# Kernel tuning notes

Measured on AMD Instinct MI355X. Metric: run time of the kernel, lower is better.

## Reference

```python
import jax, jax.numpy as jnp
import numpy as np

D_IN, D_OUT, D_K, D_V, H = 768, 768, 64, 64, 12


def setup_inputs() -> dict:
    key = jax.random.key(0)
    ks = jax.random.split(key, 16)
    b, nq, nk = 4, 1024, 1024
    inp = {
        'queries': jax.random.normal(ks[0], (b, nq, D_IN), jnp.float32),
        'keys': jax.random.normal(ks[1], (b, nk, D_IN), jnp.float32),
        'values': jax.random.normal(ks[2], (b, nk, D_IN), jnp.float32),
        'loss_map': jax.random.normal(ks[3], (b, nk, H), jnp.float32),
        'attention_mask': jax.random.randint(ks[4], (b, H, nq, nk), 0, 2).astype(bool),
        'attention_weights': jax.random.uniform(ks[5], (b, H, nq, nk), jnp.float32),
        # learned params (stored as (in, out); math-equivalent to torch Linear)
        'Wq': jax.random.normal(ks[6], (D_IN, H * D_K), jnp.float32) * 0.02,
        'bq': jnp.zeros((H * D_K,), jnp.float32),
        'Wk': jax.random.normal(ks[7], (D_IN, H * D_K), jnp.float32) * 0.02,
        'bk': jnp.zeros((H * D_K,), jnp.float32),
        'Wv': jax.random.normal(ks[8], (D_IN, H * D_V), jnp.float32) * 0.02,
        'bv': jnp.zeros((H * D_V,), jnp.float32),
        'Wo': jax.random.normal(ks[9], (H * D_V, D_OUT), jnp.float32) * 0.02,
        'bo': jnp.zeros((D_OUT,), jnp.float32),
    }
    return inp


def reference(queries, keys, values, loss_map, attention_mask, attention_weights,
              Wq, bq, Wk, bk, Wv, bv, Wo, bo):
    b, nq, _ = queries.shape
    nk = keys.shape[1]
    # projections -> (b, h, n, d)
    q = (queries @ Wq + bq).reshape(b, nq, H, D_K).transpose(0, 2, 1, 3)
    k = (keys @ Wk + bk).reshape(b, nk, H, D_K).transpose(0, 2, 1, 3)
    v = (values @ Wv + bv).reshape(b, nk, H, D_V).transpose(0, 2, 1, 3)
    # scaled scores (b, h, nq, nk)
    att = jnp.einsum('bhqd,bhkd->bhqk', q, k) / np.sqrt(D_K).astype(np.float32)
    att = att * attention_weights
    att = jnp.where(attention_mask, -jnp.inf, att)
    # additive per-key, per-head bias: loss_map (b, nk, h) -> (b, h, 1, nk)
    w_g = loss_map.transpose(0, 2, 1)[:, :, None, :]
    w_mn = jax.nn.softmax(att + w_g, axis=-1)
    # dropout is identity in eval / p=0
    out = jnp.einsum('bhqk,bhkd->bhqd', w_mn, v)
    out = out.transpose(0, 2, 1, 3).reshape(b, nq, H * D_V)
    return out @ Wo + bo
```

## Files before the change

### kernel.cpp

```cpp
#include <hip/hip_runtime.h>
#include <hip/hip_bf16.h>
#include <hip/hip_fp16.h>
#include <cmath>

static constexpr int HN = 12;
static constexpr int DHEAD = 64;
static constexpr int DMODEL = 768;
static constexpr int NQ = 1024;
static constexpr int NB = 4;
static constexpr int NCH = 4;
static constexpr int MROWS = NB * NQ;
static constexpr size_t PER = (size_t)NB * HN * NQ * DHEAD;
static constexpr size_t WN  = (size_t)DMODEL * DMODEL;
static constexpr size_t CHROWS = (size_t)NB * HN * NQ;

typedef __attribute__((ext_vector_type(8))) short bf16x8;
typedef __attribute__((ext_vector_type(4))) float f32x4;

static __device__ __forceinline__ unsigned short f2bf(float f) {
    unsigned int u = __builtin_bit_cast(unsigned int, f);
    unsigned int r = (u + 0x7FFFu + ((u >> 16) & 1u)) >> 16;
    return (unsigned short)r;
}
static __device__ __forceinline__ unsigned pack2(float lo, float hi) {
    return (unsigned)f2bf(lo) | ((unsigned)f2bf(hi) << 16);
}
static __device__ __forceinline__ unsigned short f2h(float f) {
    return __half_as_ushort(__float2half(f));
}

typedef const __attribute__((address_space(1))) unsigned int gu32;
typedef __attribute__((address_space(3))) unsigned int lu32;
static __device__ __forceinline__ void gload16(const void* g, void* l) {
    __builtin_amdgcn_global_load_lds((gu32*)g, (lu32*)l, 16, 0, 0);
}

__global__ __launch_bounds__(256)
void cvt3(const float* __restrict__ a, const float* __restrict__ b, const float* __restrict__ c,
          unsigned short* __restrict__ oa, unsigned short* __restrict__ ob, unsigned short* __restrict__ oc)
{
    const int z = blockIdx.z;
    const float* s = z == 0 ? a : z == 1 ? b : c;
    unsigned short* d = z == 0 ? oa : z == 1 ? ob : oc;
    size_t i = ((size_t)blockIdx.x * 256 + threadIdx.x) * 4;
    float4 v = *(const float4*)&s[i];
    ushort4 u;
    u.x = f2bf(v.x); u.y = f2bf(v.y); u.z = f2bf(v.z); u.w = f2bf(v.w);
    *(ushort4*)&d[i] = u;
}

__global__ __launch_bounds__(256)
void wtrans(const float* __restrict__ w0, const float* __restrict__ w1,
            const float* __restrict__ w2, const float* __restrict__ w3,
            unsigned short* __restrict__ o0, unsigned short* __restrict__ o1,
            unsigned short* __restrict__ o2, unsigned short* __restrict__ o3)
{
    const int z = blockIdx.z;
    const float* in = z == 0 ? w0 : z == 1 ? w1 : z == 2 ? w2 : w3;
    unsigned short* out = z == 0 ? o0 : z == 1 ? o1 : z == 2 ? o2 : o3;
    __shared__ float t[64][65];
    const int tid = threadIdx.x;
    const int k0 = blockIdx.x * 64, n0 = blockIdx.y * 64;
    #pragma unroll
    for (int l = 0; l < 16; ++l) {
        int idx = l * 256 + tid, r = idx >> 6, cc = idx & 63;
        t[r][cc] = in[(size_t)(k0 + r) * DMODEL + n0 + cc];
    }
    __syncthreads();
    #pragma unroll
    for (int l = 0; l < 16; ++l) {
        int idx = l * 256 + tid, r = idx >> 6, cc = idx & 63;
        out[(size_t)(n0 + r) * DMODEL + k0 + cc] = f2bf(t[cc][r]);
    }
}

static __device__ __forceinline__
void gemm_body(const unsigned short* __restrict__ A, const unsigned short* __restrict__ Wt,
               const float* __restrict__ bias, void* __restrict__ C, int layout)
{
    constexpr int K = DMODEL;
    __shared__ unsigned short As[128 * 64];
    __shared__ unsigned short Bs[128 * 64];
    const int tid = threadIdx.x, w = tid >> 6, lane = tid & 63;
    const int c = lane & 15, g = lane >> 4;
    const int wr = w >> 1, wc = w & 1;
    const int bn = blockIdx.x * 128, bm = blockIdx.y * 128;

    f32x4 acc[4][4] = {};
    for (int k0 = 0; k0 < K; k0 += 64) {
        #pragma unroll
        for (int it = 0; it < 4; ++it) {
            int idx = it * 256 + tid, r = idx >> 3, blk = idx & 7;
            int so = (blk ^ (r & 7)) << 3;
            gload16(A  + (size_t)(bm + r) * K + k0 + so, &As[(it * 256 + w * 64) * 8]);
            gload16(Wt + (size_t)(bn + r) * K + k0 + so, &Bs[(it * 256 + w * 64) * 8]);
        }
        __syncthreads();
        #pragma unroll
        for (int kk = 0; kk < 2; ++kk) {
            bf16x8 a[4], b[4];
            #pragma unroll
            for (int mi = 0; mi < 4; ++mi) {
                int row = wr * 64 + mi * 16 + c;
                a[mi] = *(const bf16x8*)&As[row * 64 + ((((kk << 2) | g) ^ (row & 7)) << 3)];
            }
            #pragma unroll
            for (int ni = 0; ni < 4; ++ni) {
                int row = wc * 64 + ni * 16 + c;
                b[ni] = *(const bf16x8*)&Bs[row * 64 + ((((kk << 2) | g) ^ (row & 7)) << 3)];
            }
            #pragma unroll
            for (int mi = 0; mi < 4; ++mi)
                #pragma unroll
                for (int ni = 0; ni < 4; ++ni)
                    acc[mi][ni] = __builtin_amdgcn_mfma_f32_16x16x32_bf16(a[mi], b[ni], acc[mi][ni], 0, 0, 0);
        }
        __syncthreads();
    }

    #pragma unroll
    for (int ni = 0; ni < 4; ++ni) {
        int col = bn + wc * 64 + ni * 16 + c;
        float bvx = bias[col];
        int hh = col >> 6, d = col & 63;
        #pragma unroll
        for (int mi = 0; mi < 4; ++mi) {
            int m0 = bm + wr * 64 + mi * 16 + 4 * g;
            int bb = m0 >> 10, nn0 = m0 & (NQ - 1);
            if (layout == 0) {
                float* o = (float*)C;
                #pragma unroll
                for (int j = 0; j < 4; ++j)
                    o[(size_t)(m0 + j) * DMODEL + col] = acc[mi][ni][j] + bvx;
            } else if (layout == 1) {
                unsigned short* o = (unsigned short*)C;
                #pragma unroll
                for (int j = 0; j < 4; ++j)
                    o[(((size_t)bb * HN + hh) * NQ + nn0 + j) * DHEAD + d] =
                        f2bf(acc[mi][ni][j] + bvx);
            } else {
                unsigned short* o = (unsigned short*)C;
                ushort4 u;
                u.x = f2bf(acc[mi][ni][0] + bvx);
                u.y = f2bf(acc[mi][ni][1] + bvx);
                u.z = f2bf(acc[mi][ni][2] + bvx);
                u.w = f2bf(acc[mi][ni][3] + bvx);
                *(ushort4*)&o[(((size_t)bb * HN + hh) * DHEAD + d) * NQ + nn0] = u;
            }
        }
    }
}

__global__ __launch_bounds__(256)
void qkv_gemm(const unsigned short* __restrict__ qa, const unsigned short* __restrict__ ka,
              const unsigned short* __restrict__ va,
              const unsigned short* __restrict__ wq, const unsigned short* __restrict__ wk,
              const unsigned short* __restrict__ wv,
              const float* __restrict__ bq, const float* __restrict__ bk, const float* __restrict__ bv,
              unsigned short* __restrict__ qo, unsigned short* __restrict__ ko,
              unsigned short* __restrict__ vo)
{
    const int z = blockIdx.z;
    const unsigned short* A  = z == 0 ? qa : z == 1 ? ka : va;
    const unsigned short* Wt = z == 0 ? wq : z == 1 ? wk : wv;
    const float* bias        = z == 0 ? bq : z == 1 ? bk : bv;
    unsigned short* C        = z == 0 ? qo : z == 1 ? ko : vo;
    gemm_body(A, Wt, bias, C, z == 2 ? 2 : 1);
}

__global__ __launch_bounds__(256)
void o_gemm(const unsigned short* __restrict__ A, const unsigned short* __restrict__ Wt,
            const float* __restrict__ bias, float* __restrict__ C)
{
    gemm_body(A, Wt, bias, C, 0);
}

__global__ __launch_bounds__(256, 5)
void attn_part(const unsigned short* __restrict__ qws,
               const unsigned short* __restrict__ kws,
               const unsigned short* __restrict__ vtws,
               const float* __restrict__ aw, const int* __restrict__ mask,
               const float* __restrict__ lm,
               unsigned short* __restrict__ opart, float* __restrict__ mpart,
               float* __restrict__ lpart)
{
    const int qt = blockIdx.x, h = blockIdx.y;
    const int b = blockIdx.z >> 2, ch = blockIdx.z & 3;
    const int tid = threadIdx.x;
    const int w = tid >> 6, lane = tid & 63;
    const int c = lane & 15, g = lane >> 4;

    __shared__ unsigned short Ks[2][32 * 64];
    __shared__ unsigned short Vs[2][64 * 32];
    __shared__ float lms[256];

    const size_t bh = (size_t)b * HN + h;
    const unsigned short* qbase  = qws  + (bh * NQ + (size_t)qt * 64) * DHEAD;
    const unsigned short* kbase  = kws  + (bh * NQ + (size_t)ch * 256) * DHEAD;
    const unsigned short* vtbase = vtws + bh * DHEAD * NQ + ch * 256;

    auto stageKV = [&](int kt, int bufi) {
        {
            int r = tid >> 3, blk = tid & 7;
            int so = (blk ^ (r & 7)) << 3;
            gload16(kbase + (size_t)(kt * 32 + r) * DHEAD + so, &Ks[bufi][(w * 64) * 8]);
        }
        {
            int r = tid >> 2, blk = tid & 3;
            int so = ((blk ^ ((tid >> 4) & 3)) << 3);
            gload16(vtbase + (size_t)r * NQ + kt * 32 + so, &Vs[bufi][(w * 64) * 8]);
        }
    };

    const int qrow = w * 16 + c;
    const bf16x8 qf0 = *(const bf16x8*)&qbase[qrow * DHEAD + g * 8];
    const bf16x8 qf1 = *(const bf16x8*)&qbase[qrow * DHEAD + 32 + g * 8];

    const size_t awbase = (bh * NQ + (size_t)(qt * 64 + qrow)) * NQ + ch * 256;

    f32x4 O[4] = {{0,0,0,0},{0,0,0,0},{0,0,0,0},{0,0,0,0}};
    float mrun = -1e30f, lrun = 0.f;
    const int srcl = c + ((g & 1) << 5);
    const bool hiT = (g >> 1) != 0;
    const int vsw = (c >> 2);

    lms[tid] = lm[((size_t)b * NQ + ch * 256 + tid) * HN + h];
    stageKV(0, 0);
    __syncthreads();

    #pragma unroll
    for (int kt = 0; kt < 8; ++kt) {
        const int cur = kt & 1;
        if (kt < 7) stageKV(kt + 1, cur ^ 1);

        float4 aw4[2]; int4 mk4[2]; float4 lm4[2];
        #pragma unroll
        for (int nt = 0; nt < 2; ++nt) {
            size_t o = awbase + kt * 32 + nt * 16 + 4 * g;
            aw4[nt] = *(const float4*)&aw[o];
            mk4[nt] = *(const int4*)&mask[o];
            lm4[nt] = *(const float4*)&lms[kt * 32 + nt * 16 + 4 * g];
        }

        f32x4 s[2] = {{0,0,0,0},{0,0,0,0}};
        #pragma unroll
        for (int kk = 0; kk < 2; ++kk) {
            bf16x8 qf = kk ? qf1 : qf0;
            #pragma unroll
            for (int nt = 0; nt < 2; ++nt) {
                int krow = nt * 16 + c;
                bf16x8 kf = *(const bf16x8*)&Ks[cur][krow * 64 + ((((kk << 2) | g) ^ (c & 7)) << 3)];
                s[nt] = __builtin_amdgcn_mfma_f32_16x16x32_bf16(kf, qf, s[nt], 0, 0, 0);
            }
        }

        float p[2][4];
        float tmax = -INFINITY;
        #pragma unroll
        for (int nt = 0; nt < 2; ++nt) {
            const float* av = (const float*)&aw4[nt];
            const int*   mv = (const int*)&mk4[nt];
            const float* lv = (const float*)&lm4[nt];
            #pragma unroll
            for (int j = 0; j < 4; ++j) {
                float v = mv[j] ? -1e30f : fmaf(s[nt][j], 0.125f * av[j], lv[j]);
                p[nt][j] = v;
                tmax = fmaxf(tmax, v);
            }
        }
        tmax = fmaxf(tmax, __shfl_xor(tmax, 16));
        tmax = fmaxf(tmax, __shfl_xor(tmax, 32));

        float mn = fmaxf(mrun, tmax);
        float scal = __expf(mrun - mn);
        mrun = mn;
        float rs = 0.f;
        #pragma unroll
        for (int nt = 0; nt < 2; ++nt)
            #pragma unroll
            for (int j = 0; j < 4; ++j) {
                float e = __expf(p[nt][j] - mn);
                p[nt][j] = e;
                rs += e;
            }
        rs += __shfl_xor(rs, 16);
        rs += __shfl_xor(rs, 32);
        lrun = lrun * scal + rs;
        #pragma unroll
        for (int nd = 0; nd < 4; ++nd) O[nd] *= scal;

        int pk[2][2];
        #pragma unroll
        for (int nt = 0; nt < 2; ++nt) {
            pk[nt][0] = (int)pack2(p[nt][0], p[nt][1]);
            pk[nt][1] = (int)pack2(p[nt][2], p[nt][3]);
        }

        {
            int xa0 = __shfl(pk[0][0], srcl),      xb0 = __shfl(pk[1][0], srcl);
            int xa1 = __shfl(pk[0][1], srcl),      xb1 = __shfl(pk[1][1], srcl);
            int xa2 = __shfl(pk[0][0], srcl + 16), xb2 = __shfl(pk[1][0], srcl + 16);
            int xa3 = __shfl(pk[0][1], srcl + 16), xb3 = __shfl(pk[1][1], srcl + 16);
            int4 bi;
            bi.x = hiT ? xb0 : xa0;
            bi.y = hiT ? xb1 : xa1;
            bi.z = hiT ? xb2 : xa2;
            bi.w = hiT ? xb3 : xa3;
            bf16x8 pa = __builtin_bit_cast(bf16x8, bi);
            #pragma unroll
            for (int nd = 0; nd < 4; ++nd) {
                int vrow = nd * 16 + c;
                bf16x8 vf = *(const bf16x8*)&Vs[cur][vrow * 32 + ((g ^ vsw) << 3)];
                O[nd] = __builtin_amdgcn_mfma_f32_16x16x32_bf16(vf, pa, O[nd], 0, 0, 0);
            }
        }
        if (kt < 7) __syncthreads();
    }

    const size_t prow = ((size_t)(ch * NB + b) * HN + h) * NQ + qt * 64 + qrow;
    #pragma unroll
    for (int nd = 0; nd < 4; ++nd) {
        ushort4 u;
        u.x = f2h(O[nd][0]); u.y = f2h(O[nd][1]);
        u.z = f2h(O[nd][2]); u.w = f2h(O[nd][3]);
        *(ushort4*)&opart[prow * 64 + nd * 16 + 4 * g] = u;
    }
    if (g == 0) {
        mpart[prow] = mrun;
        lpart[prow] = lrun;
    }
}

__global__ __launch_bounds__(256)
void attn_combine(const unsigned short* __restrict__ opart, const float* __restrict__ mpart,
                  const float* __restrict__ lpart, unsigned short* __restrict__ out)
{
    const int qt = blockIdx.x, h = blockIdx.y, b = blockIdx.z;
    const int tid = threadIdx.x;
    const int q = qt * 64 + (tid >> 2);
    const int d0 = (tid & 3) * 16;
    const size_t row = ((size_t)b * HN + h) * NQ + q;

    float mv[4], lv[4];
    float M = -INFINITY;
    #pragma unroll
    for (int ci = 0; ci < 4; ++ci) {
        mv[ci] = mpart[ci * CHROWS + row];
        lv[ci] = lpart[ci * CHROWS + row];
        M = fmaxf(M, mv[ci]);
    }
    float L = 0.f;
    float wc[4];
    #pragma unroll
    for (int ci = 0; ci < 4; ++ci) {
        wc[ci] = __expf(mv[ci] - M);
        L += lv[ci] * wc[ci];
    }
    const float inv = 1.f / L;

    float o[16] = {};
    #pragma unroll
    for (int ci = 0; ci < 4; ++ci) {
        const unsigned short* src = opart + (ci * CHROWS + row) * 64 + d0;
        #pragma unroll
        for (int i = 0; i < 4; ++i) {
            ushort4 u = *(const ushort4*)&src[i * 4];
            o[i * 4 + 0] += wc[ci] * __half2float(__ushort_as_half(u.x));
            o[i * 4 + 1] += wc[ci] * __half2float(__ushort_as_half(u.y));
            o[i * 4 + 2] += wc[ci] * __half2float(__ushort_as_half(u.z));
            o[i * 4 + 3] += wc[ci] * __half2float(__ushort_as_half(u.w));
        }
    }
    const size_t ob = ((size_t)b * NQ + q) * DMODEL + h * DHEAD + d0;
    #pragma unroll
    for (int i = 0; i < 4; ++i) {
        ushort4 u;
        u.x = f2bf(o[i * 4 + 0] * inv);
        u.y = f2bf(o[i * 4 + 1] * inv);
        u.z = f2bf(o[i * 4 + 2] * inv);
        u.w = f2bf(o[i * 4 + 3] * inv);
        *(ushort4*)&out[ob + i * 4] = u;
    }
}

extern "C" void kernel_launch(void* const* d_in, const int* in_sizes, int n_in,
                              void* d_out, int out_size, void* d_ws, size_t ws_size,
                              hipStream_t stream)
{
    const float* queries = (const float*)d_in[0];
    const float* keys    = (const float*)d_in[1];
    const float* values  = (const float*)d_in[2];
    const float* lossmap = (const float*)d_in[3];
    const int*   mask    = (const int*)d_in[4];
    const float* aw      = (const float*)d_in[5];
    const float* Wq = (const float*)d_in[6];
    const float* bq = (const float*)d_in[7];
    const float* Wk = (const float*)d_in[8];
    const float* bk = (const float*)d_in[9];
    const float* Wv = (const float*)d_in[10];
    const float* bv = (const float*)d_in[11];
    const float* Wo = (const float*)d_in[12];
    const float* bo = (const float*)d_in[13];

    unsigned short* p = (unsigned short*)d_ws;
    unsigned short* qbf  = p; p += PER;
    unsigned short* kbf  = p; p += PER;
    unsigned short* vbf  = p; p += PER;
    unsigned short* qws  = p; p += PER;
    unsigned short* kws  = p; p += PER;
    unsigned short* vtws = p; p += PER;
    unsigned short* aobf = p; p += PER;
    unsigned short* wqt  = p; p += WN;
    unsigned short* wkt  = p; p += WN;
    unsigned short* wvt  = p; p += WN;
    unsigned short* wot  = p; p += WN;
    unsigned short* opart = p; p += (size_t)NCH * CHROWS * 64;
    float* fp = (float*)p;
    float* mpart = fp; fp += (size_t)NCH * CHROWS;
    float* lpart = fp; fp += (size_t)NCH * CHROWS;

    const int M = MROWS;
    cvt3<<<dim3((unsigned)(PER / 1024), 1, 3), 256, 0, stream>>>(queries, keys, values, qbf, kbf, vbf);
    wtrans<<<dim3(12, 12, 4), 256, 0, stream>>>(Wq, Wk, Wv, Wo, wqt, wkt, wvt, wot);
    qkv_gemm<<<dim3(DMODEL / 128, M / 128, 3), 256, 0, stream>>>(
        qbf, kbf, vbf, wqt, wkt, wvt, bq, bk, bv, qws, kws, vtws);
    attn_part<<<dim3(NQ / 64, HN, NB * NCH), 256, 0, stream>>>(
        qws, kws, vtws, aw, mask, lossmap, opart, mpart, lpart);
    attn_combine<<<dim3(NQ / 64, HN, NB), 256, 0, stream>>>(opart, mpart, lpart, aobf);
    o_gemm<<<dim3(DMODEL / 128, M / 128), 256, 0, stream>>>(aobf, wot, bo, (float*)d_out);
}
```

Before: 208.0 us.

## Stage attention weights and mask tiles through double-buffered LDS with async loads

```diff
diff --git a/kernel.cpp b/kernel.cpp
--- a/kernel.cpp
+++ b/kernel.cpp
@@ -175,7 +175,7 @@
     gemm_body(A, Wt, bias, C, 0);
 }
 
-__global__ __launch_bounds__(256, 5)
+__global__ __launch_bounds__(256, 3)
 void attn_part(const unsigned short* __restrict__ qws,
                const unsigned short* __restrict__ kws,
                const unsigned short* __restrict__ vtws,
@@ -192,6 +192,8 @@
 
     __shared__ unsigned short Ks[2][32 * 64];
     __shared__ unsigned short Vs[2][64 * 32];
+    __shared__ float awS[2][512 * 4];
+    __shared__ int   mkS[2][512 * 4];
     __shared__ float lms[256];
 
     const size_t bh = (size_t)b * HN + h;
@@ -199,7 +201,14 @@
     const unsigned short* kbase  = kws  + (bh * NQ + (size_t)ch * 256) * DHEAD;
     const unsigned short* vtbase = vtws + bh * DHEAD * NQ + ch * 256;
 
-    auto stageKV = [&](int kt, int bufi) {
+    const int sq0 = tid >> 3;
+    const int skg = (tid & 7) ^ (sq0 & 7);
+    const float* awg0 = aw + (bh * NQ + (size_t)(qt * 64 + sq0)) * NQ + ch * 256 + skg * 4;
+    const float* awg1 = aw + (bh * NQ + (size_t)(qt * 64 + sq0 + 32)) * NQ + ch * 256 + skg * 4;
+    const int*   mkg0 = mask + (bh * NQ + (size_t)(qt * 64 + sq0)) * NQ + ch * 256 + skg * 4;
+    const int*   mkg1 = mask + (bh * NQ + (size_t)(qt * 64 + sq0 + 32)) * NQ + ch * 256 + skg * 4;
+
+    auto stage = [&](int kt, int bufi) {
         {
             int r = tid >> 3, blk = tid & 7;
             int so = (blk ^ (r & 7)) << 3;
@@ -210,37 +219,40 @@
             int so = ((blk ^ ((tid >> 4) & 3)) << 3);
             gload16(vtbase + (size_t)r * NQ + kt * 32 + so, &Vs[bufi][(w * 64) * 8]);
         }
+        gload16(awg0 + kt * 32, &awS[bufi][(w * 64) * 4]);
+        gload16(awg1 + kt * 32, &awS[bufi][(256 + w * 64) * 4]);
+        gload16(mkg0 + kt * 32, &mkS[bufi][(w * 64) * 4]);
+        gload16(mkg1 + kt * 32, &mkS[bufi][(256 + w * 64) * 4]);
     };
 
     const int qrow = w * 16 + c;
     const bf16x8 qf0 = *(const bf16x8*)&qbase[qrow * DHEAD + g * 8];
     const bf16x8 qf1 = *(const bf16x8*)&qbase[qrow * DHEAD + 32 + g * 8];
-
-    const size_t awbase = (bh * NQ + (size_t)(qt * 64 + qrow)) * NQ + ch * 256;
 
     f32x4 O[4] = {{0,0,0,0},{0,0,0,0},{0,0,0,0},{0,0,0,0}};
     float mrun = -1e30f, lrun = 0.f;
     const int srcl = c + ((g & 1) << 5);
     const bool hiT = (g >> 1) != 0;
     const int vsw = (c >> 2);
+    const int rp0 = qrow * 8 + ((g) ^ (c & 7));
+    const int rp1 = qrow * 8 + ((4 | g) ^ (c & 7));
 
     lms[tid] = lm[((size_t)b * NQ + ch * 256 + tid) * HN + h];
-    stageKV(0, 0);
+    stage(0, 0);
     __syncthreads();
 
     #pragma unroll
     for (int kt = 0; kt < 8; ++kt) {
         const int cur = kt & 1;
-        if (kt < 7) stageKV(kt + 1, cur ^ 1);
+        if (kt < 7) stage(kt + 1, cur ^ 1);
 
         float4 aw4[2]; int4 mk4[2]; float4 lm4[2];
-        #pragma unroll
-        for (int nt = 0; nt < 2; ++nt) {
-            size_t o = awbase + kt * 32 + nt * 16 + 4 * g;
-            aw4[nt] = *(const float4*)&aw[o];
-            mk4[nt] = *(const int4*)&mask[o];
-            lm4[nt] = *(const float4*)&lms[kt * 32 + nt * 16 + 4 * g];
-        }
+        aw4[0] = *(const float4*)&awS[cur][rp0 * 4];
+        aw4[1] = *(const float4*)&awS[cur][rp1 * 4];
+        mk4[0] = *(const int4*)&mkS[cur][rp0 * 4];
+        mk4[1] = *(const int4*)&mkS[cur][rp1 * 4];
+        lm4[0] = *(const float4*)&lms[kt * 32 + 4 * g];
+        lm4[1] = *(const float4*)&lms[kt * 32 + 16 + 4 * g];
 
         f32x4 s[2] = {{0,0,0,0},{0,0,0,0}};
         #pragma unroll
```

After: 185.1 us. -11.0%, faster.

## Split attention keys into eight chunks and stage scores scale/mask in LDS

Applied to the files above, without the earlier changes.

```diff
diff --git a/kernel.cpp b/kernel.cpp
--- a/kernel.cpp
+++ b/kernel.cpp
@@ -8,7 +8,7 @@
 static constexpr int DMODEL = 768;
 static constexpr int NQ = 1024;
 static constexpr int NB = 4;
-static constexpr int NCH = 4;
+static constexpr int NCH = 8;
 static constexpr int MROWS = NB * NQ;
 static constexpr size_t PER = (size_t)NB * HN * NQ * DHEAD;
 static constexpr size_t WN  = (size_t)DMODEL * DMODEL;
@@ -27,6 +27,9 @@
 }
 static __device__ __forceinline__ unsigned short f2h(float f) {
     return __half_as_ushort(__float2half(f));
+}
+static __device__ __forceinline__ float bf2f(unsigned short u) {
+    return __builtin_bit_cast(float, (unsigned)u << 16);
 }
 
 typedef const __attribute__((address_space(1))) unsigned int gu32;
@@ -175,7 +178,7 @@
     gemm_body(A, Wt, bias, C, 0);
 }
 
-__global__ __launch_bounds__(256, 5)
+__global__ __launch_bounds__(256)
 void attn_part(const unsigned short* __restrict__ qws,
                const unsigned short* __restrict__ kws,
                const unsigned short* __restrict__ vtws,
@@ -185,38 +188,54 @@
                float* __restrict__ lpart)
 {
     const int qt = blockIdx.x, h = blockIdx.y;
-    const int b = blockIdx.z >> 2, ch = blockIdx.z & 3;
+    const int b = blockIdx.z >> 3, ch = blockIdx.z & 7;
     const int tid = threadIdx.x;
     const int w = tid >> 6, lane = tid & 63;
     const int c = lane & 15, g = lane >> 4;
 
-    __shared__ unsigned short Ks[2][32 * 64];
-    __shared__ unsigned short Vs[2][64 * 32];
-    __shared__ float lms[256];
+    __shared__ unsigned short Ks[4][32 * 64];
+    __shared__ unsigned short Vs[4][64 * 32];
+    __shared__ unsigned short awL[64 * 128];
+    __shared__ float lms[128];
 
     const size_t bh = (size_t)b * HN + h;
     const unsigned short* qbase  = qws  + (bh * NQ + (size_t)qt * 64) * DHEAD;
-    const unsigned short* kbase  = kws  + (bh * NQ + (size_t)ch * 256) * DHEAD;
-    const unsigned short* vtbase = vtws + bh * DHEAD * NQ + ch * 256;
-
-    auto stageKV = [&](int kt, int bufi) {
-        {
-            int r = tid >> 3, blk = tid & 7;
-            int so = (blk ^ (r & 7)) << 3;
-            gload16(kbase + (size_t)(kt * 32 + r) * DHEAD + so, &Ks[bufi][(w * 64) * 8]);
-        }
-        {
-            int r = tid >> 2, blk = tid & 3;
-            int so = ((blk ^ ((tid >> 4) & 3)) << 3);
-            gload16(vtbase + (size_t)r * NQ + kt * 32 + so, &Vs[bufi][(w * 64) * 8]);
-        }
-    };
+    const unsigned short* kbase  = kws  + (bh * NQ + (size_t)ch * 128) * DHEAD;
+    const unsigned short* vtbase = vtws + bh * DHEAD * NQ + ch * 128;
+
+    #pragma unroll
+    for (int nt2 = 0; nt2 < 4; ++nt2) {
+        int r = tid >> 3, blk = tid & 7;
+        gload16(kbase + (size_t)(nt2 * 32 + r) * DHEAD + ((blk ^ (r & 7)) << 3),
+                &Ks[nt2][w * 512]);
+        int rv = tid >> 2, blkv = tid & 3;
+        gload16(vtbase + (size_t)rv * NQ + nt2 * 32 + ((blkv ^ ((tid >> 4) & 3)) << 3),
+                &Vs[nt2][w * 512]);
+    }
+    if (tid < 128) lms[tid] = lm[((size_t)b * NQ + ch * 128 + tid) * HN + h];
+
+    {
+        const float* awrow = aw   + (bh * NQ + (size_t)qt * 64) * NQ + ch * 128;
+        const int*   mkrow = mask + (bh * NQ + (size_t)qt * 64) * NQ + ch * 128;
+        #pragma unroll
+        for (int p = 0; p < 8; ++p) {
+            int id = p * 256 + tid;
+            int row = id >> 5, G = id & 31;
+            size_t src = (size_t)row * NQ + G * 4;
+            float4 a4 = *(const float4*)&awrow[src];
+            int4   m4 = *(const int4*)&mkrow[src];
+            ushort4 u;
+            u.x = m4.x ? (unsigned short)0xBF80u : f2bf(0.125f * a4.x);
+            u.y = m4.y ? (unsigned short)0xBF80u : f2bf(0.125f * a4.y);
+            u.z = m4.z ? (unsigned short)0xBF80u : f2bf(0.125f * a4.z);
+            u.w = m4.w ? (unsigned short)0xBF80u : f2bf(0.125f * a4.w);
+            *(ushort4*)&awL[row * 128 + ((G ^ (row & 15)) << 2)] = u;
+        }
+    }
 
     const int qrow = w * 16 + c;
     const bf16x8 qf0 = *(const bf16x8*)&qbase[qrow * DHEAD + g * 8];
     const bf16x8 qf1 = *(const bf16x8*)&qbase[qrow * DHEAD + 32 + g * 8];
-
-    const size_t awbase = (bh * NQ + (size_t)(qt * 64 + qrow)) * NQ + ch * 256;
 
     f32x4 O[4] = {{0,0,0,0},{0,0,0,0},{0,0,0,0},{0,0,0,0}};
     float mrun = -1e30f, lrun = 0.f;
@@ -224,22 +243,16 @@
     const bool hiT = (g >> 1) != 0;
     const int vsw = (c >> 2);
 
-    lms[tid] = lm[((size_t)b * NQ + ch * 256 + tid) * HN + h];
-    stageKV(0, 0);
     __syncthreads();
 
     #pragma unroll
-    for (int kt = 0; kt < 8; ++kt) {
-        const int cur = kt & 1;
-        if (kt < 7) stageKV(kt + 1, cur ^ 1);
-
-        float4 aw4[2]; int4 mk4[2]; float4 lm4[2];
+    for (int nt2 = 0; nt2 < 4; ++nt2) {
+        ushort4 sc4[2]; float4 lm4[2];
         #pragma unroll
         for (int nt = 0; nt < 2; ++nt) {
-            size_t o = awbase + kt * 32 + nt * 16 + 4 * g;
-            aw4[nt] = *(const float4*)&aw[o];
-            mk4[nt] = *(const int4*)&mask[o];
-            lm4[nt] = *(const float4*)&lms[kt * 32 + nt * 16 + 4 * g];
+            int G = nt2 * 8 + nt * 4 + g;
+            sc4[nt] = *(const ushort4*)&awL[qrow * 128 + ((G ^ (qrow & 15)) << 2)];
+            lm4[nt] = *(const float4*)&lms[nt2 * 32 + nt * 16 + 4 * g];
         }
 
         f32x4 s[2] = {{0,0,0,0},{0,0,0,0}};
@@ -249,7 +262,7 @@
             #pragma unroll
             for (int nt = 0; nt < 2; ++nt) {
                 int krow = nt * 16 + c;
-                bf16x8 kf = *(const bf16x8*)&Ks[cur][krow * 64 + ((((kk << 2) | g) ^ (c & 7)) << 3)];
+                bf16x8 kf = *(const bf16x8*)&Ks[nt2][krow * 64 + ((((kk << 2) | g) ^ (c & 7)) << 3)];
                 s[nt] = __builtin_amdgcn_mfma_f32_16x16x32_bf16(kf, qf, s[nt], 0, 0, 0);
             }
         }
@@ -258,12 +271,12 @@
         float tmax = -INFINITY;
         #pragma unroll
         for (int nt = 0; nt < 2; ++nt) {
-            const float* av = (const float*)&aw4[nt];
-            const int*   mv = (const int*)&mk4[nt];
+            const unsigned short* su = (const unsigned short*)&sc4[nt];
             const float* lv = (const float*)&lm4[nt];
             #pragma unroll
             for (int j = 0; j < 4; ++j) {
-                float v = mv[j] ? -1e30f : fmaf(s[nt][j], 0.125f * av[j], lv[j]);
+                unsigned short u = su[j];
+                float v = (u & 0x8000u) ? -1e30f : fmaf(s[nt][j], bf2f(u), lv[j]);
                 p[nt][j] = v;
                 tmax = fmaxf(tmax, v);
             }
@@ -310,11 +323,10 @@
             #pragma unroll
             for (int nd = 0; nd < 4; ++nd) {
                 int vrow = nd * 16 + c;
-                bf16x8 vf = *(const bf16x8*)&Vs[cur][vrow * 32 + ((g ^ vsw) << 3)];
+                bf16x8 vf = *(const bf16x8*)&Vs[nt2][vrow * 32 + ((g ^ vsw) << 3)];
                 O[nd] = __builtin_amdgcn_mfma_f32_16x16x32_bf16(vf, pa, O[nd], 0, 0, 0);
             }
         }
-        if (kt < 7) __syncthreads();
     }
 
     const size_t prow = ((size_t)(ch * NB + b) * HN + h) * NQ + qt * 64 + qrow;
@@ -341,18 +353,18 @@
     const int d0 = (tid & 3) * 16;
     const size_t row = ((size_t)b * HN + h) * NQ + q;
 
-    float mv[4], lv[4];
+    float mv[NCH], lv[NCH];
     float M = -INFINITY;
     #pragma unroll
-    for (int ci = 0; ci < 4; ++ci) {
+    for (int ci = 0; ci < NCH; ++ci) {
         mv[ci] = mpart[ci * CHROWS + row];
         lv[ci] = lpart[ci * CHROWS + row];
         M = fmaxf(M, mv[ci]);
     }
     float L = 0.f;
-    float wc[4];
-    #pragma unroll
-    for (int ci = 0; ci < 4; ++ci) {
+    float wc[NCH];
+    #pragma unroll
+    for (int ci = 0; ci < NCH; ++ci) {
         wc[ci] = __expf(mv[ci] - M);
         L += lv[ci] * wc[ci];
     }
@@ -360,7 +372,7 @@
 
     float o[16] = {};
     #pragma unroll
-    for (int ci = 0; ci < 4; ++ci) {
+    for (int ci = 0; ci < NCH; ++ci) {
         const unsigned short* src = opart + (ci * CHROWS + row) * 64 + d0;
         #pragma unroll
         for (int i = 0; i < 4; ++i) {
```

Result: slower. 234.4 us (+12.7%).

## Fuse input bf16 conversion into QKV GEMM and stage attention scale/mask via LDS

Applied to the files above, without the earlier changes.

```diff
diff --git a/kernel.cpp b/kernel.cpp
--- a/kernel.cpp
+++ b/kernel.cpp
@@ -15,6 +15,7 @@
 static constexpr size_t CHROWS = (size_t)NB * HN * NQ;
 
 typedef __attribute__((ext_vector_type(8))) short bf16x8;
+typedef __attribute__((ext_vector_type(8))) short short8;
 typedef __attribute__((ext_vector_type(4))) float f32x4;
 
 static __device__ __forceinline__ unsigned short f2bf(float f) {
@@ -28,25 +29,14 @@
 static __device__ __forceinline__ unsigned short f2h(float f) {
     return __half_as_ushort(__float2half(f));
 }
+static __device__ __forceinline__ float bf2f(unsigned short u) {
+    return __builtin_bit_cast(float, (unsigned)u << 16);
+}
 
 typedef const __attribute__((address_space(1))) unsigned int gu32;
 typedef __attribute__((address_space(3))) unsigned int lu32;
 static __device__ __forceinline__ void gload16(const void* g, void* l) {
     __builtin_amdgcn_global_load_lds((gu32*)g, (lu32*)l, 16, 0, 0);
-}
-
-__global__ __launch_bounds__(256)
-void cvt3(const float* __restrict__ a, const float* __restrict__ b, const float* __restrict__ c,
-          unsigned short* __restrict__ oa, unsigned short* __restrict__ ob, unsigned short* __restrict__ oc)
-{
-    const int z = blockIdx.z;
-    const float* s = z == 0 ? a : z == 1 ? b : c;
-    unsigned short* d = z == 0 ? oa : z == 1 ? ob : oc;
-    size_t i = ((size_t)blockIdx.x * 256 + threadIdx.x) * 4;
-    float4 v = *(const float4*)&s[i];
-    ushort4 u;
-    u.x = f2bf(v.x); u.y = f2bf(v.y); u.z = f2bf(v.z); u.w = f2bf(v.w);
-    *(ushort4*)&d[i] = u;
 }
 
 __global__ __launch_bounds__(256)
@@ -74,9 +64,103 @@
     }
 }
 
-static __device__ __forceinline__
-void gemm_body(const unsigned short* __restrict__ A, const unsigned short* __restrict__ Wt,
-               const float* __restrict__ bias, void* __restrict__ C, int layout)
+__global__ __launch_bounds__(256)
+void qkv_gemm(const float* __restrict__ qa, const float* __restrict__ ka,
+              const float* __restrict__ va,
+              const unsigned short* __restrict__ wq, const unsigned short* __restrict__ wk,
+              const unsigned short* __restrict__ wv,
+              const float* __restrict__ bq, const float* __restrict__ bk, const float* __restrict__ bv,
+              unsigned short* __restrict__ qo, unsigned short* __restrict__ ko,
+              unsigned short* __restrict__ vo)
+{
+    constexpr int K = DMODEL;
+    const int z = blockIdx.z;
+    const float* A            = z == 0 ? qa : z == 1 ? ka : va;
+    const unsigned short* Wt  = z == 0 ? wq : z == 1 ? wk : wv;
+    const float* bias         = z == 0 ? bq : z == 1 ? bk : bv;
+    unsigned short* C         = z == 0 ? qo : z == 1 ? ko : vo;
+    const int layout = (z == 2) ? 2 : 1;
+
+    __shared__ unsigned short As[128 * 64];
+    __shared__ unsigned short Bs[128 * 64];
+    const int tid = threadIdx.x, w = tid >> 6, lane = tid & 63;
+    const int c = lane & 15, g = lane >> 4;
+    const int wr = w >> 1, wc = w & 1;
+    const int bn = blockIdx.x * 128, bm = blockIdx.y * 128;
+
+    f32x4 acc[4][4] = {};
+    for (int k0 = 0; k0 < K; k0 += 64) {
+        #pragma unroll
+        for (int it = 0; it < 4; ++it) {
+            int idx = it * 256 + tid, r = idx >> 3, blk = idx & 7;
+            const float* src = A + (size_t)(bm + r) * K + k0 + blk * 8;
+            float4 a0 = *(const float4*)src;
+            float4 a1 = *(const float4*)(src + 4);
+            short8 v;
+            v[0] = (short)f2bf(a0.x); v[1] = (short)f2bf(a0.y);
+            v[2] = (short)f2bf(a0.z); v[3] = (short)f2bf(a0.w);
+            v[4] = (short)f2bf(a1.x); v[5] = (short)f2bf(a1.y);
+            v[6] = (short)f2bf(a1.z); v[7] = (short)f2bf(a1.w);
+            *(short8*)&As[r * 64 + ((blk ^ (r & 7)) << 3)] = v;
+        }
+        #pragma unroll
+        for (int it = 0; it < 4; ++it) {
+            int idx = it * 256 + tid, r = idx >> 3, blk = idx & 7;
+            int so = (blk ^ (r & 7)) << 3;
+            gload16(Wt + (size_t)(bn + r) * K + k0 + so, &Bs[(it * 256 + w * 64) * 8]);
+        }
+        __syncthreads();
+        #pragma unroll
+        for (int kk = 0; kk < 2; ++kk) {
+            bf16x8 a[4], b[4];
+            #pragma unroll
+            for (int mi = 0; mi < 4; ++mi) {
+                int row = wr * 64 + mi * 16 + c;
+                a[mi] = *(const bf16x8*)&As[row * 64 + ((((kk << 2) | g) ^ (row & 7)) << 3)];
+            }
+            #pragma unroll
+            for (int ni = 0; ni < 4; ++ni) {
+                int row = wc * 64 + ni * 16 + c;
+                b[ni] = *(const bf16x8*)&Bs[row * 64 + ((((kk << 2) | g) ^ (row & 7)) << 3)];
+            }
+            #pragma unroll
+            for (int mi = 0; mi < 4; ++mi)
+                #pragma unroll
+                for (int ni = 0; ni < 4; ++ni)
+                    acc[mi][ni] = __builtin_amdgcn_mfma_f32_16x16x32_bf16(a[mi], b[ni], acc[mi][ni], 0, 0, 0);
+        }
+        __syncthreads();
+    }
+
+    #pragma unroll
+    for (int ni = 0; ni < 4; ++ni) {
+        int col = bn + wc * 64 + ni * 16 + c;
+        float bvx = bias[col];
+        int hh = col >> 6, d = col & 63;
+        #pragma unroll
+        for (int mi = 0; mi < 4; ++mi) {
+            int m0 = bm + wr * 64 + mi * 16 + 4 * g;
+            int bb = m0 >> 10, nn0 = m0 & (NQ - 1);
+            if (layout == 1) {
+                #pragma unroll
+                for (int j = 0; j < 4; ++j)
+                    C[(((size_t)bb * HN + hh) * NQ + nn0 + j) * DHEAD + d] =
+                        f2bf(acc[mi][ni][j] + bvx);
+            } else {
+                ushort4 u;
+                u.x = f2bf(acc[mi][ni][0] + bvx);
+                u.y = f2bf(acc[mi][ni][1] + bvx);
+                u.z = f2bf(acc[mi][ni][2] + bvx);
+                u.w = f2bf(acc[mi][ni][3] + bvx);
+                *(ushort4*)&C[(((size_t)bb * HN + hh) * DHEAD + d) * NQ + nn0] = u;
+            }
+        }
+    }
+}
+
+__global__ __launch_bounds__(256)
+void o_gemm(const unsigned short* __restrict__ A, const unsigned short* __restrict__ Wt,
+            const float* __restrict__ bias, float* __restrict__ C)
 {
     constexpr int K = DMODEL;
     __shared__ unsigned short As[128 * 64];
@@ -122,60 +206,17 @@
     for (int ni = 0; ni < 4; ++ni) {
         int col = bn + wc * 64 + ni * 16 + c;
         float bvx = bias[col];
-        int hh = col >> 6, d = col & 63;
         #pragma unroll
         for (int mi = 0; mi < 4; ++mi) {
             int m0 = bm + wr * 64 + mi * 16 + 4 * g;
-            int bb = m0 >> 10, nn0 = m0 & (NQ - 1);
-            if (layout == 0) {
-                float* o = (float*)C;
-                #pragma unroll
-                for (int j = 0; j < 4; ++j)
-                    o[(size_t)(m0 + j) * DMODEL + col] = acc[mi][ni][j] + bvx;
-            } else if (layout == 1) {
-                unsigned short* o = (unsigned short*)C;
-                #pragma unroll
-                for (int j = 0; j < 4; ++j)
-                    o[(((size_t)bb * HN + hh) * NQ + nn0 + j) * DHEAD + d] =
-                        f2bf(acc[mi][ni][j] + bvx);
-            } else {
-                unsigned short* o = (unsigned short*)C;
-                ushort4 u;
-                u.x = f2bf(acc[mi][ni][0] + bvx);
-                u.y = f2bf(acc[mi][ni][1] + bvx);
-                u.z = f2bf(acc[mi][ni][2] + bvx);
-                u.w = f2bf(acc[mi][ni][3] + bvx);
-                *(ushort4*)&o[(((size_t)bb * HN + hh) * DHEAD + d) * NQ + nn0] = u;
-            }
-        }
-    }
-}
-
-__global__ __launch_bounds__(256)
-void qkv_gemm(const unsigned short* __restrict__ qa, const unsigned short* __restrict__ ka,
-              const unsigned short* __restrict__ va,
-              const unsigned short* __restrict__ wq, const unsigned short* __restrict__ wk,
-              const unsigned short* __restrict__ wv,
-              const float* __restrict__ bq, const float* __restrict__ bk, const float* __restrict__ bv,
-              unsigned short* __restrict__ qo, unsigned short* __restrict__ ko,
-              unsigned short* __restrict__ vo)
-{
-    const int z = blockIdx.z;
-    const unsigned short* A  = z == 0 ? qa : z == 1 ? ka : va;
-    const unsigned short* Wt = z == 0 ? wq : z == 1 ? wk : wv;
-    const float* bias        = z == 0 ? bq : z == 1 ? bk : bv;
-    unsigned short* C        = z == 0 ? qo : z == 1 ? ko : vo;
-    gemm_body(A, Wt, bias, C, z == 2 ? 2 : 1);
-}
-
-__global__ __launch_bounds__(256)
-void o_gemm(const unsigned short* __restrict__ A, const unsigned short* __restrict__ Wt,
-            const float* __restrict__ bias, float* __restrict__ C)
-{
-    gemm_body(A, Wt, bias, C, 0);
-}
-
-__global__ __launch_bounds__(256, 5)
+            #pragma unroll
+            for (int j = 0; j < 4; ++j)
+                C[(size_t)(m0 + j) * DMODEL + col] = acc[mi][ni][j] + bvx;
+        }
+    }
+}
+
+__global__ __launch_bounds__(256, 6)
 void attn_part(const unsigned short* __restrict__ qws,
                const unsigned short* __restrict__ kws,
                const unsigned short* __restrict__ vtws,
@@ -192,6 +233,7 @@
 
     __shared__ unsigned short Ks[2][32 * 64];
     __shared__ unsigned short Vs[2][64 * 32];
+    __shared__ unsigned short scS[2][64 * 32];
     __shared__ float lms[256];
 
     const size_t bh = (size_t)b * HN + h;
@@ -199,48 +241,69 @@
     const unsigned short* kbase  = kws  + (bh * NQ + (size_t)ch * 256) * DHEAD;
     const unsigned short* vtbase = vtws + bh * DHEAD * NQ + ch * 256;
 
-    auto stageKV = [&](int kt, int bufi) {
+    const int srow = tid >> 2;
+    const int G0 = (tid & 3) * 2;
+    const float* awrow = aw   + (bh * NQ + (size_t)(qt * 64 + srow)) * NQ + ch * 256 + G0 * 4;
+    const int*   mkrow = mask + (bh * NQ + (size_t)(qt * 64 + srow)) * NQ + ch * 256 + G0 * 4;
+    const int ssw0 = ((G0     ^ (srow & 7)) * 4);
+    const int ssw1 = (((G0|1) ^ (srow & 7)) * 4);
+
+    auto stage = [&](int kt, int bufi) {
         {
             int r = tid >> 3, blk = tid & 7;
-            int so = (blk ^ (r & 7)) << 3;
-            gload16(kbase + (size_t)(kt * 32 + r) * DHEAD + so, &Ks[bufi][(w * 64) * 8]);
+            gload16(kbase + (size_t)(kt * 32 + r) * DHEAD + ((blk ^ (r & 7)) << 3),
+                    &Ks[bufi][w * 512]);
         }
         {
-            int r = tid >> 2, blk = tid & 3;
-            int so = ((blk ^ ((tid >> 4) & 3)) << 3);
-            gload16(vtbase + (size_t)r * NQ + kt * 32 + so, &Vs[bufi][(w * 64) * 8]);
+            int rv = tid >> 2, blkv = tid & 3;
+            gload16(vtbase + (size_t)rv * NQ + kt * 32 + ((blkv ^ ((tid >> 4) & 3)) << 3),
+                    &Vs[bufi][w * 512]);
+        }
+        {
+            float4 a0 = *(const float4*)&awrow[kt * 32];
+            float4 a1 = *(const float4*)&awrow[kt * 32 + 4];
+            int4   m0 = *(const int4*)&mkrow[kt * 32];
+            int4   m1 = *(const int4*)&mkrow[kt * 32 + 4];
+            ushort4 u0, u1;
+            u0.x = m0.x ? (unsigned short)0xBF80u : f2bf(0.125f * a0.x);
+            u0.y = m0.y ? (unsigned short)0xBF80u : f2bf(0.125f * a0.y);
+            u0.z = m0.z ? (unsigned short)0xBF80u : f2bf(0.125f * a0.z);
+            u0.w = m0.w ? (unsigned short)0xBF80u : f2bf(0.125f * a0.w);
+            u1.x = m1.x ? (unsigned short)0xBF80u : f2bf(0.125f * a1.x);
+            u1.y = m1.y ? (unsigned short)0xBF80u : f2bf(0.125f * a1.y);
+            u1.z = m1.z ? (unsigned short)0xBF80u : f2bf(0.125f * a1.z);
+            u1.w = m1.w ? (unsigned short)0xBF80u : f2bf(0.125f * a1.w);
+            *(ushort4*)&scS[bufi][srow * 32 + ssw0] = u0;
+            *(ushort4*)&scS[bufi][srow * 32 + ssw1] = u1;
         }
     };
 
     const int qrow = w * 16 + c;
     const bf16x8 qf0 = *(const bf16x8*)&qbase[qrow * DHEAD + g * 8];
     const bf16x8 qf1 = *(const bf16x8*)&qbase[qrow * DHEAD + 32 + g * 8];
-
-    const size_t awbase = (bh * NQ + (size_t)(qt * 64 + qrow)) * NQ + ch * 256;
 
     f32x4 O[4] = {{0,0,0,0},{0,0,0,0},{0,0,0,0},{0,0,0,0}};
     float mrun = -1e30f, lrun = 0.f;
     const int srcl = c + ((g & 1) << 5);
     const bool hiT = (g >> 1) != 0;
     const int vsw = (c >> 2);
+    const int rp0 = qrow * 32 + (((0 * 4 + g) ^ (qrow & 7)) * 4);
+    const int rp1 = qrow * 32 + (((1 * 4 + g) ^ (qrow & 7)) * 4);
 
     lms[tid] = lm[((size_t)b * NQ + ch * 256 + tid) * HN + h];
-    stageKV(0, 0);
+    stage(0, 0);
     __syncthreads();
 
     #pragma unroll
     for (int kt = 0; kt < 8; ++kt) {
         const int cur = kt & 1;
-        if (kt < 7) stageKV(kt + 1, cur ^ 1);
-
-        float4 aw4[2]; int4 mk4[2]; float4 lm4[2];
-        #pragma unroll
-        for (int nt = 0; nt < 2; ++nt) {
-            size_t o = awbase + kt * 32 + nt * 16 + 4 * g;
-            aw4[nt] = *(const float4*)&aw[o];
-            mk4[nt] = *(const int4*)&mask[o];
-            lm4[nt] = *(const float4*)&lms[kt * 32 + nt * 16 + 4 * g];
-        }
+        if (kt < 7) stage(kt + 1, cur ^ 1);
+
+        ushort4 sc4[2]; float4 lm4[2];
+        sc4[0] = *(const ushort4*)&scS[cur][rp0];
+        sc4[1] = *(const ushort4*)&scS[cur][rp1];
+        lm4[0] = *(const float4*)&lms[kt * 32 + 4 * g];
+        lm4[1] = *(const float4*)&lms[kt * 32 + 16 + 4 * g];
 
         f32x4 s[2] = {{0,0,0,0},{0,0,0,0}};
         #pragma unroll
@@ -258,12 +321,12 @@
         float tmax = -INFINITY;
         #pragma unroll
         for (int nt = 0; nt < 2; ++nt) {
-            const float* av = (const float*)&aw4[nt];
-            const int*   mv = (const int*)&mk4[nt];
+            const unsigned short* su = (const unsigned short*)&sc4[nt];
             const float* lv = (const float*)&lm4[nt];
             #pragma unroll
             for (int j = 0; j < 4; ++j) {
-                float v = mv[j] ? -1e30f : fmaf(s[nt][j], 0.125f * av[j], lv[j]);
+                unsigned short u = su[j];
+                float v = (u & 0x8000u) ? -1e30f : fmaf(s[nt][j], bf2f(u), lv[j]);
                 p[nt][j] = v;
                 tmax = fmaxf(tmax, v);
             }
@@ -341,18 +404,18 @@
     const int d0 = (tid & 3) * 16;
     const size_t row = ((size_t)b * HN + h) * NQ + q;
 
-    float mv[4], lv[4];
+    float mv[NCH], lv[NCH];
     float M = -INFINITY;
     #pragma unroll
-    for (int ci = 0; ci < 4; ++ci) {
+    for (int ci = 0; ci < NCH; ++ci) {
         mv[ci] = mpart[ci * CHROWS + row];
         lv[ci] = lpart[ci * CHROWS + row];
         M = fmaxf(M, mv[ci]);
     }
     float L = 0.f;
-    float wc[4];
-    #pragma unroll
-    for (int ci = 0; ci < 4; ++ci) {
+    float wc[NCH];
+    #pragma unroll
+    for (int ci = 0; ci < NCH; ++ci) {
         wc[ci] = __expf(mv[ci] - M);
         L += lv[ci] * wc[ci];
     }
@@ -360,7 +423,7 @@
 
     float o[16] = {};
     #pragma unroll
-    for (int ci = 0; ci < 4; ++ci) {
+    for (int ci = 0; ci < NCH; ++ci) {
         const unsigned short* src = opart + (ci * CHROWS + row) * 64 + d0;
         #pragma unroll
         for (int i = 0; i < 4; ++i) {
@@ -403,9 +466,6 @@
     const float* bo = (const float*)d_in[13];
 
     unsigned short* p = (unsigned short*)d_ws;
-    unsigned short* qbf  = p; p += PER;
-    unsigned short* kbf  = p; p += PER;
-    unsigned short* vbf  = p; p += PER;
     unsigned short* qws  = p; p += PER;
     unsigned short* kws  = p; p += PER;
     unsigned short* vtws = p; p += PER;
@@ -420,10 +480,9 @@
     float* lpart = fp; fp += (size_t)NCH * CHROWS;
 
     const int M = MROWS;
-    cvt3<<<dim3((unsigned)(PER / 1024), 1, 3), 256, 0, stream>>>(queries, keys, values, qbf, kbf, vbf);
     wtrans<<<dim3(12, 12, 4), 256, 0, stream>>>(Wq, Wk, Wv, Wo, wqt, wkt, wvt, wot);
     qkv_gemm<<<dim3(DMODEL / 128, M / 128, 3), 256, 0, stream>>>(
-        qbf, kbf, vbf, wqt, wkt, wvt, bq, bk, bv, qws, kws, vtws);
+        queries, keys, values, wqt, wkt, wvt, bq, bk, bv, qws, kws, vtws);
     attn_part<<<dim3(NQ / 64, HN, NB * NCH), 256, 0, stream>>>(
         qws, kws, vtws, aw, mask, lossmap, opart, mpart, lpart);
     attn_combine<<<dim3(NQ / 64, HN, NB), 256, 0, stream>>>(opart, mpart, lpart, aobf);
```

After: 219.3 us. 5.4% more time.
